# Optimization experiments

Measured on AMD Instinct MI355X. Metric: run time of the kernel, lower is better.

## Reference

```python
import jax, jax.numpy as jnp
import numpy as np

EMBED_DIM = 1024
NUM_HEADS = 16
HEAD_DIM = EMBED_DIM // NUM_HEADS
SCALE = HEAD_DIM ** (-0.5)
CLAMP = 50000.0
MASK_FILL = -9e15


def setup_inputs() -> dict:
    key = jax.random.key(0)
    ks = jax.random.split(key, 12)
    B, Lq, Lk = 4, 1024, 1024
    q = jax.random.normal(ks[0], (B, Lq, EMBED_DIM), dtype=jnp.float32)
    k = jax.random.normal(ks[1], (B, Lk, EMBED_DIM), dtype=jnp.float32)
    v = jax.random.normal(ks[2], (B, Lk, EMBED_DIM), dtype=jnp.float32)
    attention_mask = jax.random.randint(ks[3], (B, Lk), 0, 2, dtype=jnp.int32)
    s = 0.02  # xavier-ish scale
    Wq = jax.random.normal(ks[4], (EMBED_DIM, EMBED_DIM), dtype=jnp.float32) * s
    Wk = jax.random.normal(ks[5], (EMBED_DIM, EMBED_DIM), dtype=jnp.float32) * s
    Wv = jax.random.normal(ks[6], (EMBED_DIM, EMBED_DIM), dtype=jnp.float32) * s
    Wo = jax.random.normal(ks[7], (EMBED_DIM, EMBED_DIM), dtype=jnp.float32) * s
    bq = jnp.zeros((EMBED_DIM,), jnp.float32)
    bk = jnp.zeros((EMBED_DIM,), jnp.float32)
    bv = jnp.zeros((EMBED_DIM,), jnp.float32)
    bo = jnp.zeros((EMBED_DIM,), jnp.float32)
    return {"q": q, "k": k, "v": v, "attention_mask": attention_mask,
            "Wq": Wq, "bq": bq, "Wk": Wk, "bk": bk,
            "Wv": Wv, "bv": bv, "Wo": Wo, "bo": bo}


def _split_heads(x, B, L):
    # [B, L, E] -> [B, H, L, D]
    return x.reshape(B, L, NUM_HEADS, HEAD_DIM).transpose(0, 2, 1, 3)


def reference(q, k, v, attention_mask, Wq, bq, Wk, bk, Wv, bv, Wo, bo):
    B, Lq, _ = q.shape
    Lk = k.shape[1]
    # projections (Linear: x @ W.T + b), query pre-scaled as in source
    qs = _split_heads((q @ Wq.T + bq) * SCALE, B, Lq)   # [B,H,Lq,D]
    ks = _split_heads(k @ Wk.T + bk, B, Lk)             # [B,H,Lk,D]
    vs = _split_heads(v @ Wv.T + bv, B, Lk)             # [B,H,Lk,D]
    logits = jnp.einsum('bhqd,bhkd->bhqk', qs, ks)      # [B,H,Lq,Lk]
    logits = jnp.clip(logits, -CLAMP, CLAMP)
    # mask: where 0 -> large negative, else the mask value itself is added
    m = attention_mask.astype(logits.dtype)
    madd = jnp.where(attention_mask == 0, MASK_FILL, m)[:, None, None, :]
    logits = logits + madd
    attn = jax.nn.softmax(logits, axis=-1)              # [B,H,Lq,Lk]
    out = jnp.einsum('bhqk,bhkd->bhqd', attn, vs)       # dropout is eval-mode identity
    out = out.transpose(0, 2, 1, 3).reshape(B, Lq, EMBED_DIM)
    out = out @ Wo.T + bo
    return out, attn
```

## Files before the change

kernel.cpp:

```cpp
#include <hip/hip_runtime.h>

typedef __attribute__((ext_vector_type(8))) short s16x8;
typedef __attribute__((ext_vector_type(4))) short s16x4;
typedef __attribute__((ext_vector_type(4))) float f32x4;

#define DEVI __device__ __forceinline__

DEVI unsigned short f2bf(float f){
  unsigned int u = __float_as_uint(f);
  return (unsigned short)((u + 0x7fffu + ((u >> 16) & 1u)) >> 16);
}
DEVI float bf2f(unsigned short h){ return __uint_as_float(((unsigned int)h) << 16); }

DEVI s16x8 mk8(s16x4 a, s16x4 b){
  s16x8 r;
  r[0]=a[0]; r[1]=a[1]; r[2]=a[2]; r[3]=a[3];
  r[4]=b[0]; r[5]=b[1]; r[6]=b[2]; r[7]=b[3];
  return r;
}

DEVI f32x4 mfma16(s16x8 a, s16x8 b, f32x4 c){
  return __builtin_amdgcn_mfma_f32_16x16x32_bf16(a, b, c, 0, 0, 0);
}

DEVI void gload16(const unsigned short* g, unsigned short* l){
  __builtin_amdgcn_global_load_lds((const __attribute__((address_space(1))) void*)g,
                                   (__attribute__((address_space(3))) void*)l, 16, 0, 0);
}

__global__ __launch_bounds__(256) void cvt_all_k(
    const float* __restrict__ q, const float* __restrict__ k, const float* __restrict__ v,
    const float* __restrict__ wq, const float* __restrict__ wk,
    const float* __restrict__ wv, const float* __restrict__ wo,
    unsigned short* __restrict__ ws)
{
  int bi = blockIdx.x, tid = threadIdx.x;
  const float* src; unsigned short* dst; int base;
  if (bi < 3072){
    int t = bi >> 10;
    src = (t==0) ? q : ((t==1) ? k : v);
    dst = ws + t*4194304;
    base = (bi & 1023) * 4096;
  } else {
    int t = (bi - 3072) >> 8;
    src = (t==0) ? wq : ((t==1) ? wk : ((t==2) ? wv : wo));
    dst = ws + 12582912 + t*1048576;
    base = ((bi - 3072) & 255) * 4096;
  }
  #pragma unroll
  for (int it = 0; it < 4; ++it){
    int i = base + it*1024 + tid*4;
    float4 f = *(const float4*)(src + i);
    s16x4 o;
    o[0] = (short)f2bf(f.x); o[1] = (short)f2bf(f.y);
    o[2] = (short)f2bf(f.z); o[3] = (short)f2bf(f.w);
    *(s16x4*)(dst + i) = o;
  }
}

__global__ __launch_bounds__(256) void proj_k(
    const unsigned short* __restrict__ Xall, const unsigned short* __restrict__ Wall,
    const float* __restrict__ bq, const float* __restrict__ bk, const float* __restrict__ bv,
    unsigned short* __restrict__ QK, unsigned short* __restrict__ Vt)
{
  __shared__ unsigned short Asm[2][4096];
  __shared__ unsigned short Bsm[2][4096];
  const int tid = threadIdx.x, lane = tid & 63;
  const int w = tid >> 6, g = lane >> 4, ln = lane & 15;
  const int z = blockIdx.z;
  const int m0 = blockIdx.y * 128, n0 = blockIdx.x * 128;
  const int wm = w >> 1, wn = w & 1;
  const unsigned short* A  = Xall + z * 4194304;
  const unsigned short* Bw = Wall + z * 1048576;
  const float* bias = (z==0) ? bq : ((z==1) ? bk : bv);

  f32x4 acc[4][4];
  #pragma unroll
  for (int i=0;i<4;++i)
    #pragma unroll
    for (int j=0;j<4;++j) acc[i][j] = (f32x4){0.f,0.f,0.f,0.f};

  auto stage = [&](int buf, int kt){
    #pragma unroll
    for (int r=0;r<2;++r){
      int c = r*256 + tid;
      int row = c >> 2, cs = (c & 3) ^ ((row >> 1) & 3);
      gload16(A + (m0+row)*1024 + kt*32 + cs*8, &Asm[buf][(r*256 + (tid & 192))*8]);
    }
    #pragma unroll
    for (int r=0;r<2;++r){
      int c = r*256 + tid;
      int row = c >> 2, cs = (c & 3) ^ ((row >> 1) & 3);
      gload16(Bw + (n0+row)*1024 + kt*32 + cs*8, &Bsm[buf][(r*256 + (tid & 192))*8]);
    }
  };

  stage(0, 0);
  for (int kt = 0; kt < 32; ++kt){
    __syncthreads();
    if (kt + 1 < 32) stage((kt+1)&1, kt+1);
    const unsigned short* As = Asm[kt&1];
    const unsigned short* Bs = Bsm[kt&1];
    s16x8 af[4], bf[4];
    #pragma unroll
    for (int mf=0; mf<4; ++mf){
      int row = wm*64 + mf*16 + ln;
      int xr = row & 6;
      const unsigned short* p = As + row*32;
      s16x4 lo = *(const s16x4*)(p + ((g ^ xr)<<2));
      s16x4 hi = *(const s16x4*)(p + (((g|4) ^ xr)<<2));
      af[mf] = mk8(lo, hi);
    }
    #pragma unroll
    for (int nf=0; nf<4; ++nf){
      int row = wn*64 + nf*16 + ln;
      int xr = row & 6;
      const unsigned short* p = Bs + row*32;
      s16x4 lo = *(const s16x4*)(p + ((g ^ xr)<<2));
      s16x4 hi = *(const s16x4*)(p + (((g|4) ^ xr)<<2));
      bf[nf] = mk8(lo, hi);
    }
    #pragma unroll
    for (int mf=0; mf<4; ++mf)
      #pragma unroll
      for (int nf=0; nf<4; ++nf)
        acc[mf][nf] = mfma16(af[mf], bf[nf], acc[mf][nf]);
  }

  if (z < 2){
    unsigned short* O = QK + z * 4194304;
    #pragma unroll
    for (int nf=0; nf<4; ++nf){
      int n = n0 + wn*64 + nf*16 + ln;
      float bv_ = bias[n];
      int hh = n >> 6, d = n & 63;
      #pragma unroll
      for (int mf=0; mf<4; ++mf){
        int mb = m0 + wm*64 + mf*16 + g*4;
        #pragma unroll
        for (int r=0;r<4;++r){
          int m = mb + r;
          int bb = m >> 10, l = m & 1023;
          float val = acc[mf][nf][r] + bv_;
          if (z == 0) val *= 0.125f;
          O[((bb*16 + hh)*1024 + l)*64 + d] = f2bf(val);
        }
      }
    }
  } else {
    #pragma unroll
    for (int nf=0; nf<4; ++nf){
      int n = n0 + wn*64 + nf*16 + ln;
      float bv_ = bias[n];
      int hh = n >> 6, d = n & 63;
      #pragma unroll
      for (int mf=0; mf<4; ++mf){
        int mb = m0 + wm*64 + mf*16 + g*4;
        int bb = mb >> 10, l = mb & 1023;
        s16x4 o;
        #pragma unroll
        for (int r=0;r<4;++r) o[r] = (short)f2bf(acc[mf][nf][r] + bv_);
        *(s16x4*)(Vt + ((bb*16 + hh)*64 + d)*1024 + l) = o;
      }
    }
  }
}

__global__ __launch_bounds__(256) void attn_k(
    const unsigned short* __restrict__ Qp, const unsigned short* __restrict__ Kp,
    const unsigned short* __restrict__ Vt, const int* __restrict__ mask,
    float* __restrict__ attn, unsigned short* __restrict__ Ob)
{
  __shared__ unsigned short P[64][1032];
  __shared__ unsigned short Qs[4096];
  __shared__ unsigned short KV[2][4096];
  __shared__ float rsi[64];

  const int tid = threadIdx.x, lane = tid & 63;
  const int w = tid >> 6, g = lane >> 4, ln = lane & 15;
  const int qt = blockIdx.x, bh = blockIdx.y, b = bh >> 4, h = bh & 15;
  const int q0 = qt * 64;

  auto stage64 = [&](unsigned short* dstbuf, const unsigned short* srcbase, int rowStride){
    #pragma unroll
    for (int r=0;r<2;++r){
      int c = r*256 + tid;
      int row = c >> 3, cs = (c & 7) ^ (row & 7);
      gload16(srcbase + row*rowStride + cs*8, dstbuf + (r*256 + (tid & 192))*8);
    }
  };

  stage64(Qs, Qp + (bh*1024 + q0)*64, 64);
  stage64(KV[0], Kp + bh*65536, 64);
  __syncthreads();

  s16x8 qf[2];
  {
    int row = w*16 + ln, xr = (row & 7) << 1;
    const unsigned short* p = Qs + row*64;
    #pragma unroll
    for (int ks=0; ks<2; ++ks){
      s16x4 lo = *(const s16x4*)(p + (((ks*8 + g) ^ xr) << 2));
      s16x4 hi = *(const s16x4*)(p + (((ks*8 + g + 4) ^ xr) << 2));
      qf[ks] = mk8(lo, hi);
    }
  }

  float rsum[4] = {0.f, 0.f, 0.f, 0.f};

  for (int kt = 0; kt < 16; ++kt){
    if (kt + 1 < 16) stage64(KV[(kt+1)&1], Kp + bh*65536 + (kt+1)*4096, 64);
    const unsigned short* Ks = KV[kt&1];
    f32x4 sacc[4];
    #pragma unroll
    for (int nf=0;nf<4;++nf) sacc[nf] = (f32x4){0.f,0.f,0.f,0.f};
    #pragma unroll
    for (int ks=0; ks<2; ++ks){
      #pragma unroll
      for (int nf=0; nf<4; ++nf){
        int row = nf*16 + ln, xr = (row & 7) << 1;
        const unsigned short* p = Ks + row*64;
        s16x4 lo = *(const s16x4*)(p + (((ks*8 + g) ^ xr) << 2));
        s16x4 hi = *(const s16x4*)(p + (((ks*8 + g + 4) ^ xr) << 2));
        sacc[nf] = mfma16(qf[ks], mk8(lo, hi), sacc[nf]);
      }
    }
    int qrow = w*16 + g*4;
    #pragma unroll
    for (int nf=0; nf<4; ++nf){
      int key = kt*64 + nf*16 + ln;
      int mv = mask[b*1024 + key];
      float ma = (float)mv;
      #pragma unroll
      for (int r=0;r<4;++r){
        float s = sacc[nf][r];
        s = fminf(fmaxf(s, -50000.f), 50000.f);
        float pv = (mv == 0) ? 0.f : __expf(s + ma);
        rsum[r] += pv;
        P[qrow + r][key] = f2bf(pv);
      }
    }
    __syncthreads();
  }

  #pragma unroll
  for (int r=0;r<4;++r){
    float s = rsum[r];
    s += __shfl_xor(s, 1); s += __shfl_xor(s, 2);
    s += __shfl_xor(s, 4); s += __shfl_xor(s, 8);
    if (ln == 0) rsi[w*16 + g*4 + r] = (s > 0.f) ? (1.f / s) : 0.f;
  }
  stage64(KV[0], Vt + bh*65536, 1024);
  __syncthreads();

  f32x4 oacc[4];
  #pragma unroll
  for (int nf=0;nf<4;++nf) oacc[nf] = (f32x4){0.f,0.f,0.f,0.f};

  for (int kt = 0; kt < 16; ++kt){
    if (kt + 1 < 16) stage64(KV[(kt+1)&1], Vt + bh*65536 + (kt+1)*64, 1024);
    const unsigned short* Vs = KV[kt&1];
    int vrow = w*16 + ln, xrv = (vrow & 7) << 1;
    const unsigned short* vp = Vs + vrow*64;
    #pragma unroll
    for (int ks=0; ks<2; ++ks){
      s16x4 lo = *(const s16x4*)(vp + (((ks*8 + g) ^ xrv) << 2));
      s16x4 hi = *(const s16x4*)(vp + (((ks*8 + g + 4) ^ xrv) << 2));
      s16x8 vf = mk8(lo, hi);
      int koff = kt*64 + ks*32;
      #pragma unroll
      for (int nf=0; nf<4; ++nf){
        const unsigned short* pp = &P[nf*16 + ln][koff + g*4];
        s16x4 plo = *(const s16x4*)(pp);
        s16x4 phi = *(const s16x4*)(pp + 16);
        oacc[nf] = mfma16(vf, mk8(plo, phi), oacc[nf]);
      }
    }
    __syncthreads();
  }

  #pragma unroll
  for (int nf=0; nf<4; ++nf){
    int qq = nf*16 + ln;
    float inv = rsi[qq];
    s16x4 o;
    #pragma unroll
    for (int r=0;r<4;++r) o[r] = (short)f2bf(oacc[nf][r] * inv);
    *(s16x4*)(Ob + (b*1024 + q0 + qq)*1024 + h*64 + w*16 + g*4) = o;
  }

  for (int i = tid; i < 8192; i += 256){
    int qq = i >> 7, c = i & 127;
    s16x8 pv = *(const s16x8*)&P[qq][c*8];
    float inv = rsi[qq];
    float* dst = attn + (bh*1024 + q0 + qq)*1024 + c*8;
    float4 f0, f1;
    f0.x = bf2f((unsigned short)pv[0]) * inv;
    f0.y = bf2f((unsigned short)pv[1]) * inv;
    f0.z = bf2f((unsigned short)pv[2]) * inv;
    f0.w = bf2f((unsigned short)pv[3]) * inv;
    f1.x = bf2f((unsigned short)pv[4]) * inv;
    f1.y = bf2f((unsigned short)pv[5]) * inv;
    f1.z = bf2f((unsigned short)pv[6]) * inv;
    f1.w = bf2f((unsigned short)pv[7]) * inv;
    *(float4*)dst = f0;
    *(float4*)(dst + 4) = f1;
  }
}

__global__ __launch_bounds__(256) void outproj_k(
    const unsigned short* __restrict__ A, const unsigned short* __restrict__ Bw,
    const float* __restrict__ bias, float* __restrict__ O)
{
  __shared__ unsigned short Asm[2][4096];
  __shared__ unsigned short Bsm[2][4096];
  const int tid = threadIdx.x, lane = tid & 63;
  const int w = tid >> 6, g = lane >> 4, ln = lane & 15;
  const int m0 = blockIdx.y * 128, n0 = blockIdx.x * 128;
  const int wm = w >> 1, wn = w & 1;

  f32x4 acc[4][4];
  #pragma unroll
  for (int i=0;i<4;++i)
    #pragma unroll
    for (int j=0;j<4;++j) acc[i][j] = (f32x4){0.f,0.f,0.f,0.f};

  auto stage = [&](int buf, int kt){
    #pragma unroll
    for (int r=0;r<2;++r){
      int c = r*256 + tid;
      int row = c >> 2, cs = (c & 3) ^ ((row >> 1) & 3);
      gload16(A + (m0+row)*1024 + kt*32 + cs*8, &Asm[buf][(r*256 + (tid & 192))*8]);
    }
    #pragma unroll
    for (int r=0;r<2;++r){
      int c = r*256 + tid;
      int row = c >> 2, cs = (c & 3) ^ ((row >> 1) & 3);
      gload16(Bw + (n0+row)*1024 + kt*32 + cs*8, &Bsm[buf][(r*256 + (tid & 192))*8]);
    }
  };

  stage(0, 0);
  for (int kt = 0; kt < 32; ++kt){
    __syncthreads();
    if (kt + 1 < 32) stage((kt+1)&1, kt+1);
    const unsigned short* As = Asm[kt&1];
    const unsigned short* Bs = Bsm[kt&1];
    s16x8 af[4], bf[4];
    #pragma unroll
    for (int mf=0; mf<4; ++mf){
      int row = wm*64 + mf*16 + ln;
      int xr = row & 6;
      const unsigned short* p = As + row*32;
      s16x4 lo = *(const s16x4*)(p + ((g ^ xr)<<2));
      s16x4 hi = *(const s16x4*)(p + (((g|4) ^ xr)<<2));
      af[mf] = mk8(lo, hi);
    }
    #pragma unroll
    for (int nf=0; nf<4; ++nf){
      int row = wn*64 + nf*16 + ln;
      int xr = row & 6;
      const unsigned short* p = Bs + row*32;
      s16x4 lo = *(const s16x4*)(p + ((g ^ xr)<<2));
      s16x4 hi = *(const s16x4*)(p + (((g|4) ^ xr)<<2));
      bf[nf] = mk8(lo, hi);
    }
    #pragma unroll
    for (int mf=0; mf<4; ++mf)
      #pragma unroll
      for (int nf=0; nf<4; ++nf)
        acc[mf][nf] = mfma16(af[mf], bf[nf], acc[mf][nf]);
  }

  #pragma unroll
  for (int nf=0; nf<4; ++nf){
    int n = n0 + wn*64 + nf*16 + ln;
    float bv_ = bias[n];
    #pragma unroll
    for (int mf=0; mf<4; ++mf){
      int mb = m0 + wm*64 + mf*16 + g*4;
      #pragma unroll
      for (int r=0;r<4;++r)
        O[(mb + r)*1024 + n] = acc[mf][nf][r] + bv_;
    }
  }
}

extern "C" void kernel_launch(void* const* d_in, const int* in_sizes, int n_in,
                              void* d_out, int out_size, void* d_ws, size_t ws_size,
                              hipStream_t stream) {
  (void)in_sizes; (void)n_in; (void)out_size; (void)ws_size;
  const float* q  = (const float*)d_in[0];
  const float* k  = (const float*)d_in[1];
  const float* v  = (const float*)d_in[2];
  const int* mask = (const int*)d_in[3];
  const float* Wq = (const float*)d_in[4];  const float* bq = (const float*)d_in[5];
  const float* Wk = (const float*)d_in[6];  const float* bk = (const float*)d_in[7];
  const float* Wv = (const float*)d_in[8];  const float* bv = (const float*)d_in[9];
  const float* Wo = (const float*)d_in[10]; const float* bo = (const float*)d_in[11];

  unsigned short* ws = (unsigned short*)d_ws;
  unsigned short* xb   = ws;
  unsigned short* wb   = ws + 12582912;
  unsigned short* Qp   = ws + 16777216;
  unsigned short* Vtb  = ws + 25165824;
  unsigned short* Ob   = ws;

  float* outp  = (float*)d_out;
  float* attnp = outp + 4194304;

  cvt_all_k<<<4096, 256, 0, stream>>>(q, k, v, Wq, Wk, Wv, Wo, ws);
  proj_k<<<dim3(8, 32, 3), 256, 0, stream>>>(xb, wb, bq, bk, bv, Qp, Vtb);
  attn_k<<<dim3(16, 64), 256, 0, stream>>>(Qp, Qp + 4194304, Vtb, mask, attnp, Ob);
  outproj_k<<<dim3(8, 32), 256, 0, stream>>>(Ob, wb + 3145728, bo, outp);
}
```

Before: 559.5 us.

## Recompute QK logits in a second pass instead of staging P in LDS

```diff
diff --git a/kernel.cpp b/kernel.cpp
--- a/kernel.cpp
+++ b/kernel.cpp
@@ -10,7 +10,6 @@
   unsigned int u = __float_as_uint(f);
   return (unsigned short)((u + 0x7fffu + ((u >> 16) & 1u)) >> 16);
 }
-DEVI float bf2f(unsigned short h){ return __uint_as_float(((unsigned int)h) << 16); }
 
 DEVI s16x8 mk8(s16x4 a, s16x4 b){
   s16x8 r;
@@ -101,7 +100,7 @@
     if (kt + 1 < 32) stage((kt+1)&1, kt+1);
     const unsigned short* As = Asm[kt&1];
     const unsigned short* Bs = Bsm[kt&1];
-    s16x8 af[4], bf[4];
+    s16x8 af[4], bfr[4];
     #pragma unroll
     for (int mf=0; mf<4; ++mf){
       int row = wm*64 + mf*16 + ln;
@@ -118,33 +117,42 @@
       const unsigned short* p = Bs + row*32;
       s16x4 lo = *(const s16x4*)(p + ((g ^ xr)<<2));
       s16x4 hi = *(const s16x4*)(p + (((g|4) ^ xr)<<2));
-      bf[nf] = mk8(lo, hi);
-    }
-    #pragma unroll
-    for (int mf=0; mf<4; ++mf)
-      #pragma unroll
-      for (int nf=0; nf<4; ++nf)
-        acc[mf][nf] = mfma16(af[mf], bf[nf], acc[mf][nf]);
+      bfr[nf] = mk8(lo, hi);
+    }
+    if (z < 2){
+      #pragma unroll
+      for (int i=0; i<4; ++i)
+        #pragma unroll
+        for (int j=0; j<4; ++j)
+          acc[i][j] = mfma16(bfr[i], af[j], acc[i][j]);
+    } else {
+      #pragma unroll
+      for (int i=0; i<4; ++i)
+        #pragma unroll
+        for (int j=0; j<4; ++j)
+          acc[i][j] = mfma16(af[i], bfr[j], acc[i][j]);
+    }
   }
 
   if (z < 2){
     unsigned short* O = QK + z * 4194304;
     #pragma unroll
-    for (int nf=0; nf<4; ++nf){
-      int n = n0 + wn*64 + nf*16 + ln;
-      float bv_ = bias[n];
-      int hh = n >> 6, d = n & 63;
-      #pragma unroll
-      for (int mf=0; mf<4; ++mf){
-        int mb = m0 + wm*64 + mf*16 + g*4;
+    for (int i=0; i<4; ++i){
+      int fb = n0 + wn*64 + i*16 + g*4;
+      f32x4 b4 = *(const f32x4*)&bias[fb];
+      int hh = fb >> 6, d = fb & 63;
+      #pragma unroll
+      for (int j=0; j<4; ++j){
+        int token = m0 + wm*64 + j*16 + ln;
+        int bb = token >> 10, l = token & 1023;
+        s16x4 o;
         #pragma unroll
         for (int r=0;r<4;++r){
-          int m = mb + r;
-          int bb = m >> 10, l = m & 1023;
-          float val = acc[mf][nf][r] + bv_;
+          float val = acc[i][j][r] + b4[r];
           if (z == 0) val *= 0.125f;
-          O[((bb*16 + hh)*1024 + l)*64 + d] = f2bf(val);
+          o[r] = (short)f2bf(val);
         }
+        *(s16x4*)(&O[((bb*16 + hh)*1024 + l)*64 + d]) = o;
       }
     }
   } else {
@@ -171,10 +179,10 @@
     const unsigned short* __restrict__ Vt, const int* __restrict__ mask,
     float* __restrict__ attn, unsigned short* __restrict__ Ob)
 {
-  __shared__ unsigned short P[64][1032];
   __shared__ unsigned short Qs[4096];
-  __shared__ unsigned short KV[2][4096];
-  __shared__ float rsi[64];
+  __shared__ unsigned short Ks[2][4096];
+  __shared__ unsigned short Vs[2][4096];
+  __shared__ float madd[1024];
 
   const int tid = threadIdx.x, lane = tid & 63;
   const int w = tid >> 6, g = lane >> 4, ln = lane & 15;
@@ -191,7 +199,16 @@
   };
 
   stage64(Qs, Qp + (bh*1024 + q0)*64, 64);
-  stage64(KV[0], Kp + bh*65536, 64);
+  stage64(Ks[0], Kp + bh*65536, 64);
+  {
+    int4 mv = *(const int4*)(mask + b*1024 + tid*4);
+    f32x4 md;
+    md[0] = mv.x ? (float)mv.x : -9e15f;
+    md[1] = mv.y ? (float)mv.y : -9e15f;
+    md[2] = mv.z ? (float)mv.z : -9e15f;
+    md[3] = mv.w ? (float)mv.w : -9e15f;
+    *(f32x4*)(&madd[tid*4]) = md;
+  }
   __syncthreads();
 
   s16x8 qf[2];
@@ -206,11 +223,10 @@
     }
   }
 
-  float rsum[4] = {0.f, 0.f, 0.f, 0.f};
-
+  float rsum = 0.f;
   for (int kt = 0; kt < 16; ++kt){
-    if (kt + 1 < 16) stage64(KV[(kt+1)&1], Kp + bh*65536 + (kt+1)*4096, 64);
-    const unsigned short* Ks = KV[kt&1];
+    if (kt + 1 < 16) stage64(Ks[(kt+1)&1], Kp + bh*65536 + (kt+1)*4096, 64);
+    const unsigned short* Kc = Ks[kt&1];
     f32x4 sacc[4];
     #pragma unroll
     for (int nf=0;nf<4;++nf) sacc[nf] = (f32x4){0.f,0.f,0.f,0.f};
@@ -219,92 +235,95 @@
       #pragma unroll
       for (int nf=0; nf<4; ++nf){
         int row = nf*16 + ln, xr = (row & 7) << 1;
-        const unsigned short* p = Ks + row*64;
+        const unsigned short* p = Kc + row*64;
         s16x4 lo = *(const s16x4*)(p + (((ks*8 + g) ^ xr) << 2));
         s16x4 hi = *(const s16x4*)(p + (((ks*8 + g + 4) ^ xr) << 2));
-        sacc[nf] = mfma16(qf[ks], mk8(lo, hi), sacc[nf]);
-      }
-    }
-    int qrow = w*16 + g*4;
+        sacc[nf] = mfma16(mk8(lo, hi), qf[ks], sacc[nf]);
+      }
+    }
     #pragma unroll
     for (int nf=0; nf<4; ++nf){
-      int key = kt*64 + nf*16 + ln;
-      int mv = mask[b*1024 + key];
-      float ma = (float)mv;
+      f32x4 md = *(const f32x4*)&madd[kt*64 + nf*16 + g*4];
       #pragma unroll
       for (int r=0;r<4;++r){
-        float s = sacc[nf][r];
-        s = fminf(fmaxf(s, -50000.f), 50000.f);
-        float pv = (mv == 0) ? 0.f : __expf(s + ma);
-        rsum[r] += pv;
-        P[qrow + r][key] = f2bf(pv);
+        float s = fminf(fmaxf(sacc[nf][r], -50000.f), 50000.f);
+        rsum += __expf(s + md[r]);
       }
     }
     __syncthreads();
   }
-
-  #pragma unroll
-  for (int r=0;r<4;++r){
-    float s = rsum[r];
-    s += __shfl_xor(s, 1); s += __shfl_xor(s, 2);
-    s += __shfl_xor(s, 4); s += __shfl_xor(s, 8);
-    if (ln == 0) rsi[w*16 + g*4 + r] = (s > 0.f) ? (1.f / s) : 0.f;
-  }
-  stage64(KV[0], Vt + bh*65536, 1024);
+  rsum += __shfl_xor(rsum, 16);
+  rsum += __shfl_xor(rsum, 32);
+  const float inv = (rsum > 0.f) ? (1.f / rsum) : 0.f;
+
+  stage64(Ks[0], Kp + bh*65536, 64);
+  stage64(Vs[0], Vt + bh*65536, 1024);
   __syncthreads();
 
   f32x4 oacc[4];
   #pragma unroll
-  for (int nf=0;nf<4;++nf) oacc[nf] = (f32x4){0.f,0.f,0.f,0.f};
+  for (int dt=0;dt<4;++dt) oacc[dt] = (f32x4){0.f,0.f,0.f,0.f};
+
+  float* arow = attn + (bh*1024 + q0 + w*16 + ln)*1024;
 
   for (int kt = 0; kt < 16; ++kt){
-    if (kt + 1 < 16) stage64(KV[(kt+1)&1], Vt + bh*65536 + (kt+1)*64, 1024);
-    const unsigned short* Vs = KV[kt&1];
-    int vrow = w*16 + ln, xrv = (vrow & 7) << 1;
-    const unsigned short* vp = Vs + vrow*64;
+    if (kt + 1 < 16){
+      stage64(Ks[(kt+1)&1], Kp + bh*65536 + (kt+1)*4096, 64);
+      stage64(Vs[(kt+1)&1], Vt + bh*65536 + (kt+1)*64, 1024);
+    }
+    const unsigned short* Kc = Ks[kt&1];
+    const unsigned short* Vc = Vs[kt&1];
+    f32x4 sacc[4];
+    #pragma unroll
+    for (int nf=0;nf<4;++nf) sacc[nf] = (f32x4){0.f,0.f,0.f,0.f};
     #pragma unroll
     for (int ks=0; ks<2; ++ks){
-      s16x4 lo = *(const s16x4*)(vp + (((ks*8 + g) ^ xrv) << 2));
-      s16x4 hi = *(const s16x4*)(vp + (((ks*8 + g + 4) ^ xrv) << 2));
-      s16x8 vf = mk8(lo, hi);
-      int koff = kt*64 + ks*32;
       #pragma unroll
       for (int nf=0; nf<4; ++nf){
-        const unsigned short* pp = &P[nf*16 + ln][koff + g*4];
-        s16x4 plo = *(const s16x4*)(pp);
-        s16x4 phi = *(const s16x4*)(pp + 16);
-        oacc[nf] = mfma16(vf, mk8(plo, phi), oacc[nf]);
+        int row = nf*16 + ln, xr = (row & 7) << 1;
+        const unsigned short* p = Kc + row*64;
+        s16x4 lo = *(const s16x4*)(p + (((ks*8 + g) ^ xr) << 2));
+        s16x4 hi = *(const s16x4*)(p + (((ks*8 + g + 4) ^ xr) << 2));
+        sacc[nf] = mfma16(mk8(lo, hi), qf[ks], sacc[nf]);
+      }
+    }
+    s16x4 pb[4];
+    #pragma unroll
+    for (int nf=0; nf<4; ++nf){
+      f32x4 md = *(const f32x4*)&madd[kt*64 + nf*16 + g*4];
+      f32x4 av;
+      #pragma unroll
+      for (int r=0;r<4;++r){
+        float s = fminf(fmaxf(sacc[nf][r], -50000.f), 50000.f);
+        float p = __expf(s + md[r]);
+        pb[nf][r] = (short)f2bf(p);
+        av[r] = p * inv;
+      }
+      *(f32x4*)(arow + kt*64 + nf*16 + g*4) = av;
+    }
+    s16x8 pf0 = mk8(pb[0], pb[1]);
+    s16x8 pf1 = mk8(pb[2], pb[3]);
+    #pragma unroll
+    for (int ks=0; ks<2; ++ks){
+      s16x8 pfc = ks ? pf1 : pf0;
+      #pragma unroll
+      for (int dt=0; dt<4; ++dt){
+        int row = dt*16 + ln, xr = (row & 7) << 1;
+        const unsigned short* vp = Vc + row*64;
+        s16x4 lo = *(const s16x4*)(vp + (((ks*8 + g) ^ xr) << 2));
+        s16x4 hi = *(const s16x4*)(vp + (((ks*8 + g + 4) ^ xr) << 2));
+        oacc[dt] = mfma16(mk8(lo, hi), pfc, oacc[dt]);
       }
     }
     __syncthreads();
   }
 
   #pragma unroll
-  for (int nf=0; nf<4; ++nf){
-    int qq = nf*16 + ln;
-    float inv = rsi[qq];
+  for (int dt=0; dt<4; ++dt){
     s16x4 o;
     #pragma unroll
-    for (int r=0;r<4;++r) o[r] = (short)f2bf(oacc[nf][r] * inv);
-    *(s16x4*)(Ob + (b*1024 + q0 + qq)*1024 + h*64 + w*16 + g*4) = o;
-  }
-
-  for (int i = tid; i < 8192; i += 256){
-    int qq = i >> 7, c = i & 127;
-    s16x8 pv = *(const s16x8*)&P[qq][c*8];
-    float inv = rsi[qq];
-    float* dst = attn + (bh*1024 + q0 + qq)*1024 + c*8;
-    float4 f0, f1;
-    f0.x = bf2f((unsigned short)pv[0]) * inv;
-    f0.y = bf2f((unsigned short)pv[1]) * inv;
-    f0.z = bf2f((unsigned short)pv[2]) * inv;
-    f0.w = bf2f((unsigned short)pv[3]) * inv;
-    f1.x = bf2f((unsigned short)pv[4]) * inv;
-    f1.y = bf2f((unsigned short)pv[5]) * inv;
-    f1.z = bf2f((unsigned short)pv[6]) * inv;
-    f1.w = bf2f((unsigned short)pv[7]) * inv;
-    *(float4*)dst = f0;
-    *(float4*)(dst + 4) = f1;
+    for (int r=0;r<4;++r) o[r] = (short)f2bf(oacc[dt][r] * inv);
+    *(s16x4*)(Ob + (b*1024 + q0 + w*16 + ln)*1024 + h*64 + dt*16 + g*4) = o;
   }
 }
 
@@ -346,7 +365,7 @@
     if (kt + 1 < 32) stage((kt+1)&1, kt+1);
     const unsigned short* As = Asm[kt&1];
     const unsigned short* Bs = Bsm[kt&1];
-    s16x8 af[4], bf[4];
+    s16x8 af[4], bfr[4];
     #pragma unroll
     for (int mf=0; mf<4; ++mf){
       int row = wm*64 + mf*16 + ln;
@@ -363,25 +382,26 @@
       const unsigned short* p = Bs + row*32;
       s16x4 lo = *(const s16x4*)(p + ((g ^ xr)<<2));
       s16x4 hi = *(const s16x4*)(p + (((g|4) ^ xr)<<2));
-      bf[nf] = mk8(lo, hi);
-    }
-    #pragma unroll
-    for (int mf=0; mf<4; ++mf)
-      #pragma unroll
-      for (int nf=0; nf<4; ++nf)
-        acc[mf][nf] = mfma16(af[mf], bf[nf], acc[mf][nf]);
-  }
-
-  #pragma unroll
-  for (int nf=0; nf<4; ++nf){
-    int n = n0 + wn*64 + nf*16 + ln;
-    float bv_ = bias[n];
-    #pragma unroll
-    for (int mf=0; mf<4; ++mf){
-      int mb = m0 + wm*64 + mf*16 + g*4;
-      #pragma unroll
-      for (int r=0;r<4;++r)
-        O[(mb + r)*1024 + n] = acc[mf][nf][r] + bv_;
+      bfr[nf] = mk8(lo, hi);
+    }
+    #pragma unroll
+    for (int i=0; i<4; ++i)
+      #pragma unroll
+      for (int j=0; j<4; ++j)
+        acc[i][j] = mfma16(bfr[i], af[j], acc[i][j]);
+  }
+
+  #pragma unroll
+  for (int i=0; i<4; ++i){
+    int fb = n0 + wn*64 + i*16 + g*4;
+    f32x4 b4 = *(const f32x4*)&bias[fb];
+    #pragma unroll
+    for (int j=0; j<4; ++j){
+      int token = m0 + wm*64 + j*16 + ln;
+      f32x4 ov;
+      #pragma unroll
+      for (int r=0;r<4;++r) ov[r] = acc[i][j][r] + b4[r];
+      *(f32x4*)(&O[token*1024 + fb]) = ov;
     }
   }
 }
```

Result: faster. 515.1 us (-7.9%).
